# Kernel optimization log

Measured on AMD Instinct MI355X. Metric: run time of the kernel, lower is better.

## Reference

```python
import jax, jax.numpy as jnp
import numpy as np

DIM = 256
HEADS = 8
DIM_HEAD = 32
WS = 8  # window_size
INNER = HEADS * DIM_HEAD
SCALE = DIM_HEAD ** -0.5


def _rel_indices():
    # (WS^2, WS^2, 2) relative position indices, shifted to be non-negative
    idx = np.array([[x, y] for x in range(WS) for y in range(WS)])
    rel = idx[None, :, :] - idx[:, None, :] + (WS - 1)
    return jnp.asarray(rel, dtype=jnp.int32)


def setup_inputs() -> dict:
    key = jax.random.key(0)
    k1, k2, k3, k4 = jax.random.split(key, 4)
    x = jax.random.normal(k1, (2, 4, 128, 128, DIM), dtype=jnp.float32)
    w_qkv = jax.random.normal(k2, (DIM, 3 * INNER), dtype=jnp.float32) * 0.02
    pos_emb = jax.random.normal(k3, (2 * WS - 1, 2 * WS - 1), dtype=jnp.float32)
    w_out = jax.random.normal(k4, (INNER, DIM), dtype=jnp.float32) * 0.02
    b_out = jnp.zeros((DIM,), dtype=jnp.float32)
    return {"x": x, "w_qkv": w_qkv, "pos_emb": pos_emb, "w_out": w_out, "b_out": b_out}


def reference(x, w_qkv, pos_emb, w_out, b_out):
    B, L, H, W, C = x.shape
    nh, nw = H // WS, W // WS
    qkv = x @ w_qkv  # (B,L,H,W,3*INNER)
    q, k, v = jnp.split(qkv, 3, axis=-1)

    def to_windows(t):
        # (B,L,H,W,INNER) -> (B,L,m,nh*nw,WS*WS,DIM_HEAD)
        t = t.reshape(B, L, nh, WS, nw, WS, HEADS, DIM_HEAD)
        t = t.transpose(0, 1, 6, 2, 4, 3, 5, 7)
        return t.reshape(B, L, HEADS, nh * nw, WS * WS, DIM_HEAD)

    q, k, v = to_windows(q), to_windows(k), to_windows(v)

    rel = _rel_indices()
    bias = pos_emb[rel[..., 0], rel[..., 1]]  # (WS^2, WS^2)

    dots = jnp.einsum('blmhic,blmhjc->blmhij', q, k) * SCALE + bias
    attn = jax.nn.softmax(dots, axis=-1)
    out = jnp.einsum('blmhij,blmhjc->blmhic', attn, v)

    # inverse window rearrange: (B,L,m,nh*nw,WS*WS,c) -> (B,L,H,W,INNER)
    out = out.reshape(B, L, HEADS, nh, nw, WS, WS, DIM_HEAD)
    out = out.transpose(0, 1, 3, 5, 4, 6, 2, 7).reshape(B, L, H, W, INNER)
    return out @ w_out + b_out
```

## Files before the change

kernel.cpp:

```cpp
#include <hip/hip_runtime.h>
#include <hip/hip_bf16.h>


typedef __attribute__((ext_vector_type(8))) short bf16x8;
typedef __attribute__((ext_vector_type(4))) float f32x4;

__device__ __forceinline__ f32x4 mfma16(bf16x8 a, bf16x8 b, f32x4 c) {
  return __builtin_amdgcn_mfma_f32_16x16x32_bf16(a, b, c, 0, 0, 0);
}

__device__ __forceinline__ unsigned short f2bf(float f) {
  __hip_bfloat16 h = __float2bfloat16(f);
  return *reinterpret_cast<unsigned short*>(&h);
}

__device__ __forceinline__ uint2 pack4(float a, float b, float c, float d) {
  union { unsigned short u[4]; uint2 v; } pk;
  pk.u[0] = f2bf(a); pk.u[1] = f2bf(b); pk.u[2] = f2bf(c); pk.u[3] = f2bf(d);
  return pk.v;
}

#define LOG2E 1.4426950408889634f
#define EXPSCALE (0.17677669529663687f * 1.4426950408889634f)

#define XO  264
#define RTS 40
#define PS  72
#define RT_ELEMS 1280
#define OFF_RT 16896
#define SMEM_ELTS 22016

__global__ void prep_kernel(const float* __restrict__ w_qkv,
                            const float* __restrict__ w_out,
                            const float* __restrict__ pos_emb,
                            unsigned short* __restrict__ wqkvT,
                            unsigned short* __restrict__ woutT,
                            float* __restrict__ bias64) {
  const int stride = gridDim.x * blockDim.x;
  const int tid = blockIdx.x * blockDim.x + threadIdx.x;
  for (int i = tid; i < 768 * 256; i += stride) {
    int n = i >> 8, k = i & 255;
    int off = ((((n >> 4) * 8 + (k >> 5)) * 4 + ((k >> 3) & 3)) * 16 + (n & 15)) * 8 + (k & 7);
    wqkvT[off] = f2bf(w_qkv[k * 768 + n]);
  }
  for (int i = tid; i < 256 * 256; i += stride) {
    int n = i >> 8, k = i & 255;
    int off = ((((n >> 4) * 8 + (k >> 5)) * 4 + ((k >> 3) & 3)) * 16 + (n & 15)) * 8 + (k & 7);
    woutT[off] = f2bf(w_out[k * 256 + n]);
  }
  for (int i = tid; i < 64 * 64; i += stride) {
    int a = i >> 6, b = i & 63;
    int d0 = (b >> 3) - (a >> 3) + 7;
    int d1 = (b & 7) - (a & 7) + 7;
    bias64[i] = pos_emb[d0 * 15 + d1] * LOG2E;
  }
}

template <bool SWAP>
__device__ __forceinline__ void gemm32(f32x4 (&acc)[4][2],
                                       const unsigned short* __restrict__ a_lds,
                                       const unsigned short* __restrict__ wT,
                                       int col0, int l15, int lq) {
  const f32x4 zero4 = {0.f, 0.f, 0.f, 0.f};
#pragma unroll
  for (int rt = 0; rt < 4; ++rt)
#pragma unroll
    for (int ct = 0; ct < 2; ++ct) acc[rt][ct] = zero4;
#pragma unroll
  for (int kk = 0; kk < 8; ++kk) {
    bf16x8 a[4], b[2];
#pragma unroll
    for (int rt = 0; rt < 4; ++rt)
      a[rt] = *(const bf16x8*)&a_lds[(rt * 16 + l15) * XO + kk * 32 + lq * 8];
#pragma unroll
    for (int ct = 0; ct < 2; ++ct)
      b[ct] = *(const bf16x8*)&wT[((((col0 >> 4) + ct) * 8 + kk) * 4 + lq) * 128 + l15 * 8];
#pragma unroll
    for (int rt = 0; rt < 4; ++rt)
#pragma unroll
      for (int ct = 0; ct < 2; ++ct)
        acc[rt][ct] = SWAP ? mfma16(b[ct], a[rt], acc[rt][ct])
                           : mfma16(a[rt], b[ct], acc[rt][ct]);
  }
}

__global__ __launch_bounds__(256, 3)
void winattn_kernel(const float* __restrict__ x,
                    const unsigned short* __restrict__ wqkvT,
                    const unsigned short* __restrict__ woutT,
                    const float* __restrict__ bias64,
                    const float* __restrict__ b_out,
                    float* __restrict__ out) {
  __shared__ unsigned short smem[SMEM_ELTS];

  const int tid = threadIdx.x;
  const int lane = tid & 63;
  const int w = tid >> 6;
  const int l15 = lane & 15;
  const int lq = lane >> 4;

  const int bid = blockIdx.x;
  const int win = bid & 255;
  const int img = bid >> 8;
  const int wy = win >> 4, wx = win & 15;

  unsigned short* x_lds  = smem;
  unsigned short* oh_lds = smem;
  unsigned short* rt_buf = smem + OFF_RT + w * RT_ELEMS;

  const f32x4 zero4 = {0.f, 0.f, 0.f, 0.f};
  const size_t img_base = (size_t)img * 128 * 128 * 256;

  {
#pragma unroll
    for (int r = 0; r < 16; ++r) {
      int p = r * 4 + w;
      const float* src = x + img_base +
          (((size_t)(wy * 8 + (p >> 3)) * 128) + (wx * 8 + (p & 7))) * 256 + lane * 4;
      float4 v4 = *(const float4*)src;
      *(uint2*)&x_lds[p * XO + lane * 4] = pack4(v4.x, v4.y, v4.z, v4.w);
    }
  }
  __syncthreads();

  bf16x8 qf[4][2], kf[4][2], vf[2][2][2];
  {
    f32x4 acc[4][2];
#pragma unroll
    for (int hh = 0; hh < 2; ++hh) {
      gemm32<true>(acc, x_lds, wqkvT, w * 64 + hh * 32, l15, lq);
#pragma unroll
      for (int h2 = 0; h2 < 2; ++h2) {
#pragma unroll
        for (int rr = 0; rr < 2; ++rr)
#pragma unroll
          for (int ct = 0; ct < 2; ++ct)
            *(uint2*)&rt_buf[(rr * 16 + l15) * RTS + ct * 16 + lq * 4] =
                pack4(acc[h2 * 2 + rr][ct][0], acc[h2 * 2 + rr][ct][1],
                      acc[h2 * 2 + rr][ct][2], acc[h2 * 2 + rr][ct][3]);
#pragma unroll
        for (int rr = 0; rr < 2; ++rr)
          qf[h2 * 2 + rr][hh] = *(const bf16x8*)&rt_buf[(rr * 16 + l15) * RTS + lq * 8];
      }
    }
#pragma unroll
    for (int hh = 0; hh < 2; ++hh) {
      gemm32<true>(acc, x_lds, wqkvT, 256 + w * 64 + hh * 32, l15, lq);
#pragma unroll
      for (int h2 = 0; h2 < 2; ++h2) {
#pragma unroll
        for (int rr = 0; rr < 2; ++rr)
#pragma unroll
          for (int ct = 0; ct < 2; ++ct)
            *(uint2*)&rt_buf[(rr * 16 + l15) * RTS + ct * 16 + lq * 4] =
                pack4(acc[h2 * 2 + rr][ct][0], acc[h2 * 2 + rr][ct][1],
                      acc[h2 * 2 + rr][ct][2], acc[h2 * 2 + rr][ct][3]);
#pragma unroll
        for (int rr = 0; rr < 2; ++rr)
          kf[h2 * 2 + rr][hh] = *(const bf16x8*)&rt_buf[(rr * 16 + l15) * RTS + lq * 8];
      }
    }
#pragma unroll
    for (int hh = 0; hh < 2; ++hh) {
      gemm32<false>(acc, x_lds, wqkvT, 512 + w * 64 + hh * 32, l15, lq);
#pragma unroll
      for (int h2 = 0; h2 < 2; ++h2) {
#pragma unroll
        for (int rr = 0; rr < 2; ++rr)
#pragma unroll
          for (int ct = 0; ct < 2; ++ct)
            *(uint2*)&rt_buf[(ct * 16 + l15) * RTS + rr * 16 + lq * 4] =
                pack4(acc[h2 * 2 + rr][ct][0], acc[h2 * 2 + rr][ct][1],
                      acc[h2 * 2 + rr][ct][2], acc[h2 * 2 + rr][ct][3]);
#pragma unroll
        for (int ft = 0; ft < 2; ++ft)
          vf[ft][h2][hh] = *(const bf16x8*)&rt_buf[(ft * 16 + l15) * RTS + lq * 8];
      }
    }
  }
  __syncthreads();

#pragma unroll
  for (int it = 0; it < 4; ++it) {
    f32x4 bias4[4];
#pragma unroll
    for (int jt = 0; jt < 4; ++jt)
      bias4[jt] = *(const f32x4*)&bias64[(it * 16 + l15) * 64 + jt * 16 + lq * 4];
#pragma unroll
    for (int hh = 0; hh < 2; ++hh) {
      f32x4 s[4];
#pragma unroll
      for (int jt = 0; jt < 4; ++jt)
        s[jt] = mfma16(kf[jt][hh], qf[it][hh], zero4);
      float rs = 0.f;
#pragma unroll
      for (int jt = 0; jt < 4; ++jt)
#pragma unroll
        for (int r = 0; r < 4; ++r) {
          s[jt][r] = __builtin_amdgcn_exp2f(s[jt][r] * EXPSCALE + bias4[jt][r]);
          rs += s[jt][r];
        }
      rs += __shfl_xor(rs, 16);
      rs += __shfl_xor(rs, 32);
      const float rinv = __builtin_amdgcn_rcpf(rs);

#pragma unroll
      for (int jt = 0; jt < 4; ++jt)
        *(uint2*)&rt_buf[l15 * PS + jt * 16 + lq * 4] =
            pack4(s[jt][0], s[jt][1], s[jt][2], s[jt][3]);
      const bf16x8 ap0 = *(const bf16x8*)&rt_buf[l15 * PS + lq * 8];
      const bf16x8 ap1 = *(const bf16x8*)&rt_buf[l15 * PS + 32 + lq * 8];

      f32x4 o0 = mfma16(vf[0][0][hh], ap0, zero4);
      o0 = mfma16(vf[0][1][hh], ap1, o0);
      f32x4 o1 = mfma16(vf[1][0][hh], ap0, zero4);
      o1 = mfma16(vf[1][1][hh], ap1, o1);

      *(uint2*)&oh_lds[(it * 16 + l15) * XO + w * 64 + hh * 32 + lq * 4] =
          pack4(o0[0] * rinv, o0[1] * rinv, o0[2] * rinv, o0[3] * rinv);
      *(uint2*)&oh_lds[(it * 16 + l15) * XO + w * 64 + hh * 32 + 16 + lq * 4] =
          pack4(o1[0] * rinv, o1[1] * rinv, o1[2] * rinv, o1[3] * rinv);
    }
  }
  __syncthreads();

  {
    f32x4 ACC[4][4];
#pragma unroll
    for (int rt = 0; rt < 4; ++rt)
#pragma unroll
      for (int ct = 0; ct < 4; ++ct) ACC[rt][ct] = zero4;
#pragma unroll
    for (int kk = 0; kk < 8; ++kk) {
      bf16x8 a[4], b[4];
#pragma unroll
      for (int rt = 0; rt < 4; ++rt)
        a[rt] = *(const bf16x8*)&oh_lds[(rt * 16 + l15) * XO + kk * 32 + lq * 8];
#pragma unroll
      for (int ct = 0; ct < 4; ++ct)
        b[ct] = *(const bf16x8*)&woutT[(((w * 4 + ct) * 8 + kk) * 4 + lq) * 128 + l15 * 8];
#pragma unroll
      for (int rt = 0; rt < 4; ++rt)
#pragma unroll
        for (int ct = 0; ct < 4; ++ct)
          ACC[rt][ct] = mfma16(b[ct], a[rt], ACC[rt][ct]);
    }
#pragma unroll
    for (int rt = 0; rt < 4; ++rt) {
      const int p = rt * 16 + l15;
      float* orow = out + img_base +
          (((size_t)(wy * 8 + (p >> 3)) * 128) + (wx * 8 + (p & 7))) * 256;
#pragma unroll
      for (int ct = 0; ct < 4; ++ct) {
        const int n0 = w * 64 + ct * 16 + lq * 4;
        const f32x4 bo4 = *(const f32x4*)&b_out[n0];
        f32x4 st;
#pragma unroll
        for (int r = 0; r < 4; ++r) st[r] = ACC[rt][ct][r] + bo4[r];
        *(f32x4*)(orow + n0) = st;
      }
    }
  }
}

extern "C" void kernel_launch(void* const* d_in, const int* in_sizes, int n_in,
                              void* d_out, int out_size, void* d_ws, size_t ws_size,
                              hipStream_t stream) {
  const float* x       = (const float*)d_in[0];
  const float* w_qkv   = (const float*)d_in[1];
  const float* pos_emb = (const float*)d_in[2];
  const float* w_out   = (const float*)d_in[3];
  const float* b_out   = (const float*)d_in[4];
  float* out = (float*)d_out;

  unsigned short* wqkvT = (unsigned short*)d_ws;
  unsigned short* woutT = wqkvT + 768 * 256;
  float* bias64 = (float*)(woutT + 256 * 256);

  prep_kernel<<<96, 256, 0, stream>>>(w_qkv, w_out, pos_emb, wqkvT, woutT, bias64);
  winattn_kernel<<<2048, 256, 0, stream>>>(x, wqkvT, woutT, bias64, b_out, out);
}
```

Baseline: 116.6 us.

## Software-pipeline QKV, attention and output-projection stages within each warp

Interleaves the QKV GEMMs with the register-transpose stores of the previous GEMM using two accumulator sets. The attention loop now computes the next tile's scores and softmax while the current P@V runs. The output projection double-buffers its A/B fragment loads one k-step ahead. The goal is to hide LDS and global load latency behind MFMA work, at the cost of more live registers and possibly lower occupancy or spills.

```diff
diff --git a/kernel.cpp b/kernel.cpp
--- a/kernel.cpp
+++ b/kernel.cpp
@@ -124,90 +124,96 @@
   __syncthreads();
 
   bf16x8 qf[4][2], kf[4][2], vf[2][2][2];
+
+#define RT_QK(ACCV, DEST, HH)                                                   \
+  _Pragma("unroll")                                                             \
+  for (int h2 = 0; h2 < 2; ++h2) {                                              \
+    _Pragma("unroll")                                                           \
+    for (int rr = 0; rr < 2; ++rr)                                              \
+      _Pragma("unroll")                                                         \
+      for (int ct = 0; ct < 2; ++ct)                                            \
+        *(uint2*)&rt_buf[(rr * 16 + l15) * RTS + ct * 16 + lq * 4] =            \
+            pack4(ACCV[h2 * 2 + rr][ct][0], ACCV[h2 * 2 + rr][ct][1],           \
+                  ACCV[h2 * 2 + rr][ct][2], ACCV[h2 * 2 + rr][ct][3]);          \
+    _Pragma("unroll")                                                           \
+    for (int rr = 0; rr < 2; ++rr)                                              \
+      DEST[h2 * 2 + rr][HH] =                                                   \
+          *(const bf16x8*)&rt_buf[(rr * 16 + l15) * RTS + lq * 8];              \
+  }
+
+#define RT_V(ACCV, HH)                                                          \
+  _Pragma("unroll")                                                             \
+  for (int h2 = 0; h2 < 2; ++h2) {                                              \
+    _Pragma("unroll")                                                           \
+    for (int rr = 0; rr < 2; ++rr)                                              \
+      _Pragma("unroll")                                                         \
+      for (int ct = 0; ct < 2; ++ct)                                            \
+        *(uint2*)&rt_buf[(ct * 16 + l15) * RTS + rr * 16 + lq * 4] =            \
+            pack4(ACCV[h2 * 2 + rr][ct][0], ACCV[h2 * 2 + rr][ct][1],           \
+                  ACCV[h2 * 2 + rr][ct][2], ACCV[h2 * 2 + rr][ct][3]);          \
+    _Pragma("unroll")                                                           \
+    for (int ft = 0; ft < 2; ++ft)                                              \
+      vf[ft][h2][HH] =                                                          \
+          *(const bf16x8*)&rt_buf[(ft * 16 + l15) * RTS + lq * 8];              \
+  }
+
   {
-    f32x4 acc[4][2];
-#pragma unroll
-    for (int hh = 0; hh < 2; ++hh) {
-      gemm32<true>(acc, x_lds, wqkvT, w * 64 + hh * 32, l15, lq);
-#pragma unroll
-      for (int h2 = 0; h2 < 2; ++h2) {
-#pragma unroll
-        for (int rr = 0; rr < 2; ++rr)
-#pragma unroll
-          for (int ct = 0; ct < 2; ++ct)
-            *(uint2*)&rt_buf[(rr * 16 + l15) * RTS + ct * 16 + lq * 4] =
-                pack4(acc[h2 * 2 + rr][ct][0], acc[h2 * 2 + rr][ct][1],
-                      acc[h2 * 2 + rr][ct][2], acc[h2 * 2 + rr][ct][3]);
-#pragma unroll
-        for (int rr = 0; rr < 2; ++rr)
-          qf[h2 * 2 + rr][hh] = *(const bf16x8*)&rt_buf[(rr * 16 + l15) * RTS + lq * 8];
-      }
-    }
-#pragma unroll
-    for (int hh = 0; hh < 2; ++hh) {
-      gemm32<true>(acc, x_lds, wqkvT, 256 + w * 64 + hh * 32, l15, lq);
-#pragma unroll
-      for (int h2 = 0; h2 < 2; ++h2) {
-#pragma unroll
-        for (int rr = 0; rr < 2; ++rr)
-#pragma unroll
-          for (int ct = 0; ct < 2; ++ct)
-            *(uint2*)&rt_buf[(rr * 16 + l15) * RTS + ct * 16 + lq * 4] =
-                pack4(acc[h2 * 2 + rr][ct][0], acc[h2 * 2 + rr][ct][1],
-                      acc[h2 * 2 + rr][ct][2], acc[h2 * 2 + rr][ct][3]);
-#pragma unroll
-        for (int rr = 0; rr < 2; ++rr)
-          kf[h2 * 2 + rr][hh] = *(const bf16x8*)&rt_buf[(rr * 16 + l15) * RTS + lq * 8];
-      }
-    }
-#pragma unroll
-    for (int hh = 0; hh < 2; ++hh) {
-      gemm32<false>(acc, x_lds, wqkvT, 512 + w * 64 + hh * 32, l15, lq);
-#pragma unroll
-      for (int h2 = 0; h2 < 2; ++h2) {
-#pragma unroll
-        for (int rr = 0; rr < 2; ++rr)
-#pragma unroll
-          for (int ct = 0; ct < 2; ++ct)
-            *(uint2*)&rt_buf[(ct * 16 + l15) * RTS + rr * 16 + lq * 4] =
-                pack4(acc[h2 * 2 + rr][ct][0], acc[h2 * 2 + rr][ct][1],
-                      acc[h2 * 2 + rr][ct][2], acc[h2 * 2 + rr][ct][3]);
-#pragma unroll
-        for (int ft = 0; ft < 2; ++ft)
-          vf[ft][h2][hh] = *(const bf16x8*)&rt_buf[(ft * 16 + l15) * RTS + lq * 8];
-      }
-    }
+    f32x4 accA[4][2], accB[4][2];
+    gemm32<true >(accA, x_lds, wqkvT,       w * 64 +  0, l15, lq);
+    gemm32<true >(accB, x_lds, wqkvT, 256 + w * 64 +  0, l15, lq);
+    RT_QK(accA, qf, 0)
+    gemm32<true >(accA, x_lds, wqkvT,       w * 64 + 32, l15, lq);
+    RT_QK(accB, kf, 0)
+    gemm32<true >(accB, x_lds, wqkvT, 256 + w * 64 + 32, l15, lq);
+    RT_QK(accA, qf, 1)
+    gemm32<false>(accA, x_lds, wqkvT, 512 + w * 64 +  0, l15, lq);
+    RT_QK(accB, kf, 1)
+    gemm32<false>(accB, x_lds, wqkvT, 512 + w * 64 + 32, l15, lq);
+    RT_V(accA, 0)
+    RT_V(accB, 1)
   }
   __syncthreads();
 
-#pragma unroll
-  for (int it = 0; it < 4; ++it) {
-    f32x4 bias4[4];
-#pragma unroll
-    for (int jt = 0; jt < 4; ++jt)
-      bias4[jt] = *(const f32x4*)&bias64[(it * 16 + l15) * 64 + jt * 16 + lq * 4];
-#pragma unroll
-    for (int hh = 0; hh < 2; ++hh) {
-      f32x4 s[4];
-#pragma unroll
-      for (int jt = 0; jt < 4; ++jt)
-        s[jt] = mfma16(kf[jt][hh], qf[it][hh], zero4);
-      float rs = 0.f;
-#pragma unroll
-      for (int jt = 0; jt < 4; ++jt)
-#pragma unroll
-        for (int r = 0; r < 4; ++r) {
-          s[jt][r] = __builtin_amdgcn_exp2f(s[jt][r] * EXPSCALE + bias4[jt][r]);
-          rs += s[jt][r];
-        }
-      rs += __shfl_xor(rs, 16);
-      rs += __shfl_xor(rs, 32);
-      const float rinv = __builtin_amdgcn_rcpf(rs);
-
+#define COMPUTE_S(IT, HH, SV, RV)                                               \
+  {                                                                             \
+    f32x4 bias4[4];                                                             \
+    _Pragma("unroll")                                                           \
+    for (int jt = 0; jt < 4; ++jt)                                              \
+      bias4[jt] = *(const f32x4*)&bias64[((IT) * 16 + l15) * 64 + jt * 16 + lq * 4]; \
+    float rs = 0.f;                                                             \
+    _Pragma("unroll")                                                           \
+    for (int jt = 0; jt < 4; ++jt) {                                            \
+      SV[jt] = mfma16(kf[jt][HH], qf[IT][HH], zero4);                           \
+      _Pragma("unroll")                                                         \
+      for (int r = 0; r < 4; ++r) {                                             \
+        SV[jt][r] = __builtin_amdgcn_exp2f(SV[jt][r] * EXPSCALE + bias4[jt][r]);\
+        rs += SV[jt][r];                                                        \
+      }                                                                         \
+    }                                                                           \
+    rs += __shfl_xor(rs, 16);                                                   \
+    rs += __shfl_xor(rs, 32);                                                   \
+    RV = __builtin_amdgcn_rcpf(rs);                                             \
+  }
+
+  {
+    f32x4 s[4];
+    float rinv;
+    COMPUTE_S(0, 0, s, rinv)
+#pragma unroll
+    for (int i = 0; i < 8; ++i) {
+      const int it = i >> 1, hh = i & 1;
 #pragma unroll
       for (int jt = 0; jt < 4; ++jt)
         *(uint2*)&rt_buf[l15 * PS + jt * 16 + lq * 4] =
             pack4(s[jt][0], s[jt][1], s[jt][2], s[jt][3]);
+
+      f32x4 sn[4];
+      float rinvn = 0.f;
+      if (i < 7) {
+        const int itn = (i + 1) >> 1, hhn = (i + 1) & 1;
+        COMPUTE_S(itn, hhn, sn, rinvn)
+      }
+
       const bf16x8 ap0 = *(const bf16x8*)&rt_buf[l15 * PS + lq * 8];
       const bf16x8 ap1 = *(const bf16x8*)&rt_buf[l15 * PS + 32 + lq * 8];
 
@@ -220,6 +226,12 @@
           pack4(o0[0] * rinv, o0[1] * rinv, o0[2] * rinv, o0[3] * rinv);
       *(uint2*)&oh_lds[(it * 16 + l15) * XO + w * 64 + hh * 32 + 16 + lq * 4] =
           pack4(o1[0] * rinv, o1[1] * rinv, o1[2] * rinv, o1[3] * rinv);
+
+      if (i < 7) {
+#pragma unroll
+        for (int jt = 0; jt < 4; ++jt) s[jt] = sn[jt];
+        rinv = rinvn;
+      }
     }
   }
   __syncthreads();
@@ -230,21 +242,33 @@
     for (int rt = 0; rt < 4; ++rt)
 #pragma unroll
       for (int ct = 0; ct < 4; ++ct) ACC[rt][ct] = zero4;
+
+    bf16x8 ag[2][4], bg[2][4];
+#pragma unroll
+    for (int rt = 0; rt < 4; ++rt)
+      ag[0][rt] = *(const bf16x8*)&oh_lds[(rt * 16 + l15) * XO + lq * 8];
+#pragma unroll
+    for (int ct = 0; ct < 4; ++ct)
+      bg[0][ct] = *(const bf16x8*)&woutT[(((w * 4 + ct) * 8 + 0) * 4 + lq) * 128 + l15 * 8];
+
 #pragma unroll
     for (int kk = 0; kk < 8; ++kk) {
-      bf16x8 a[4], b[4];
+      const int c = kk & 1, n = c ^ 1;
+      if (kk < 7) {
+#pragma unroll
+        for (int rt = 0; rt < 4; ++rt)
+          ag[n][rt] = *(const bf16x8*)&oh_lds[(rt * 16 + l15) * XO + (kk + 1) * 32 + lq * 8];
+#pragma unroll
+        for (int ct = 0; ct < 4; ++ct)
+          bg[n][ct] = *(const bf16x8*)&woutT[(((w * 4 + ct) * 8 + kk + 1) * 4 + lq) * 128 + l15 * 8];
+      }
 #pragma unroll
       for (int rt = 0; rt < 4; ++rt)
-        a[rt] = *(const bf16x8*)&oh_lds[(rt * 16 + l15) * XO + kk * 32 + lq * 8];
-#pragma unroll
-      for (int ct = 0; ct < 4; ++ct)
-        b[ct] = *(const bf16x8*)&woutT[(((w * 4 + ct) * 8 + kk) * 4 + lq) * 128 + l15 * 8];
-#pragma unroll
-      for (int rt = 0; rt < 4; ++rt)
 #pragma unroll
         for (int ct = 0; ct < 4; ++ct)
-          ACC[rt][ct] = mfma16(b[ct], a[rt], ACC[rt][ct]);
+          ACC[rt][ct] = mfma16(bg[c][ct], ag[c][rt], ACC[rt][ct]);
     }
+
 #pragma unroll
     for (int rt = 0; rt < 4; ++rt) {
       const int p = rt * 16 + l15;
```

New measurement: 132.3 us. 13.5% more time.

## Use eight waves per window block, one attention head per wave

Applied to the files above, without the earlier changes.

The block grows from 4 to 8 waves, so each wave handles one head (32 QKV columns per projection, 32 output columns) instead of two. Per-wave register arrays are halved and the x staging loop is split across 8 waves. More waves per window are meant to give more latency hiding and parallelism per CU. LDS grows to hold 8 per-wave scratch buffers, and launch bounds change to 512 threads, which may limit how many blocks fit on a CU.

```diff
diff --git a/kernel.cpp b/kernel.cpp
--- a/kernel.cpp
+++ b/kernel.cpp
@@ -28,7 +28,7 @@
 #define PS  72
 #define RT_ELEMS 1280
 #define OFF_RT 16896
-#define SMEM_ELTS 22016
+#define SMEM_ELTS 27136
 
 __global__ void prep_kernel(const float* __restrict__ w_qkv,
                             const float* __restrict__ w_out,
@@ -84,7 +84,7 @@
   }
 }
 
-__global__ __launch_bounds__(256, 3)
+__global__ __launch_bounds__(512, 4)
 void winattn_kernel(const float* __restrict__ x,
                     const unsigned short* __restrict__ wqkvT,
                     const unsigned short* __restrict__ woutT,
@@ -113,8 +113,8 @@
 
   {
 #pragma unroll
-    for (int r = 0; r < 16; ++r) {
-      int p = r * 4 + w;
+    for (int r = 0; r < 8; ++r) {
+      int p = r * 8 + w;
       const float* src = x + img_base +
           (((size_t)(wy * 8 + (p >> 3)) * 128) + (wx * 8 + (p & 7))) * 256 + lane * 4;
       float4 v4 = *(const float4*)src;
@@ -123,59 +123,50 @@
   }
   __syncthreads();
 
-  bf16x8 qf[4][2], kf[4][2], vf[2][2][2];
+  bf16x8 qf[4], kf[4], vf[2][2];
   {
     f32x4 acc[4][2];
-#pragma unroll
-    for (int hh = 0; hh < 2; ++hh) {
-      gemm32<true>(acc, x_lds, wqkvT, w * 64 + hh * 32, l15, lq);
-#pragma unroll
-      for (int h2 = 0; h2 < 2; ++h2) {
-#pragma unroll
-        for (int rr = 0; rr < 2; ++rr)
-#pragma unroll
-          for (int ct = 0; ct < 2; ++ct)
-            *(uint2*)&rt_buf[(rr * 16 + l15) * RTS + ct * 16 + lq * 4] =
-                pack4(acc[h2 * 2 + rr][ct][0], acc[h2 * 2 + rr][ct][1],
-                      acc[h2 * 2 + rr][ct][2], acc[h2 * 2 + rr][ct][3]);
-#pragma unroll
-        for (int rr = 0; rr < 2; ++rr)
-          qf[h2 * 2 + rr][hh] = *(const bf16x8*)&rt_buf[(rr * 16 + l15) * RTS + lq * 8];
-      }
-    }
-#pragma unroll
-    for (int hh = 0; hh < 2; ++hh) {
-      gemm32<true>(acc, x_lds, wqkvT, 256 + w * 64 + hh * 32, l15, lq);
-#pragma unroll
-      for (int h2 = 0; h2 < 2; ++h2) {
-#pragma unroll
-        for (int rr = 0; rr < 2; ++rr)
-#pragma unroll
-          for (int ct = 0; ct < 2; ++ct)
-            *(uint2*)&rt_buf[(rr * 16 + l15) * RTS + ct * 16 + lq * 4] =
-                pack4(acc[h2 * 2 + rr][ct][0], acc[h2 * 2 + rr][ct][1],
-                      acc[h2 * 2 + rr][ct][2], acc[h2 * 2 + rr][ct][3]);
-#pragma unroll
-        for (int rr = 0; rr < 2; ++rr)
-          kf[h2 * 2 + rr][hh] = *(const bf16x8*)&rt_buf[(rr * 16 + l15) * RTS + lq * 8];
-      }
-    }
-#pragma unroll
-    for (int hh = 0; hh < 2; ++hh) {
-      gemm32<false>(acc, x_lds, wqkvT, 512 + w * 64 + hh * 32, l15, lq);
-#pragma unroll
-      for (int h2 = 0; h2 < 2; ++h2) {
-#pragma unroll
-        for (int rr = 0; rr < 2; ++rr)
-#pragma unroll
-          for (int ct = 0; ct < 2; ++ct)
-            *(uint2*)&rt_buf[(ct * 16 + l15) * RTS + rr * 16 + lq * 4] =
-                pack4(acc[h2 * 2 + rr][ct][0], acc[h2 * 2 + rr][ct][1],
-                      acc[h2 * 2 + rr][ct][2], acc[h2 * 2 + rr][ct][3]);
-#pragma unroll
-        for (int ft = 0; ft < 2; ++ft)
-          vf[ft][h2][hh] = *(const bf16x8*)&rt_buf[(ft * 16 + l15) * RTS + lq * 8];
-      }
+    gemm32<true>(acc, x_lds, wqkvT, w * 32, l15, lq);
+#pragma unroll
+    for (int h2 = 0; h2 < 2; ++h2) {
+#pragma unroll
+      for (int rr = 0; rr < 2; ++rr)
+#pragma unroll
+        for (int ct = 0; ct < 2; ++ct)
+          *(uint2*)&rt_buf[(rr * 16 + l15) * RTS + ct * 16 + lq * 4] =
+              pack4(acc[h2 * 2 + rr][ct][0], acc[h2 * 2 + rr][ct][1],
+                    acc[h2 * 2 + rr][ct][2], acc[h2 * 2 + rr][ct][3]);
+#pragma unroll
+      for (int rr = 0; rr < 2; ++rr)
+        qf[h2 * 2 + rr] = *(const bf16x8*)&rt_buf[(rr * 16 + l15) * RTS + lq * 8];
+    }
+    gemm32<true>(acc, x_lds, wqkvT, 256 + w * 32, l15, lq);
+#pragma unroll
+    for (int h2 = 0; h2 < 2; ++h2) {
+#pragma unroll
+      for (int rr = 0; rr < 2; ++rr)
+#pragma unroll
+        for (int ct = 0; ct < 2; ++ct)
+          *(uint2*)&rt_buf[(rr * 16 + l15) * RTS + ct * 16 + lq * 4] =
+              pack4(acc[h2 * 2 + rr][ct][0], acc[h2 * 2 + rr][ct][1],
+                    acc[h2 * 2 + rr][ct][2], acc[h2 * 2 + rr][ct][3]);
+#pragma unroll
+      for (int rr = 0; rr < 2; ++rr)
+        kf[h2 * 2 + rr] = *(const bf16x8*)&rt_buf[(rr * 16 + l15) * RTS + lq * 8];
+    }
+    gemm32<false>(acc, x_lds, wqkvT, 512 + w * 32, l15, lq);
+#pragma unroll
+    for (int h2 = 0; h2 < 2; ++h2) {
+#pragma unroll
+      for (int rr = 0; rr < 2; ++rr)
+#pragma unroll
+        for (int ct = 0; ct < 2; ++ct)
+          *(uint2*)&rt_buf[(ct * 16 + l15) * RTS + rr * 16 + lq * 4] =
+              pack4(acc[h2 * 2 + rr][ct][0], acc[h2 * 2 + rr][ct][1],
+                    acc[h2 * 2 + rr][ct][2], acc[h2 * 2 + rr][ct][3]);
+#pragma unroll
+      for (int ft = 0; ft < 2; ++ft)
+        vf[ft][h2] = *(const bf16x8*)&rt_buf[(ft * 16 + l15) * RTS + lq * 8];
     }
   }
   __syncthreads();
@@ -186,63 +177,60 @@
 #pragma unroll
     for (int jt = 0; jt < 4; ++jt)
       bias4[jt] = *(const f32x4*)&bias64[(it * 16 + l15) * 64 + jt * 16 + lq * 4];
-#pragma unroll
-    for (int hh = 0; hh < 2; ++hh) {
-      f32x4 s[4];
-#pragma unroll
-      for (int jt = 0; jt < 4; ++jt)
-        s[jt] = mfma16(kf[jt][hh], qf[it][hh], zero4);
-      float rs = 0.f;
-#pragma unroll
-      for (int jt = 0; jt < 4; ++jt)
-#pragma unroll
-        for (int r = 0; r < 4; ++r) {
-          s[jt][r] = __builtin_amdgcn_exp2f(s[jt][r] * EXPSCALE + bias4[jt][r]);
-          rs += s[jt][r];
-        }
-      rs += __shfl_xor(rs, 16);
-      rs += __shfl_xor(rs, 32);
-      const float rinv = __builtin_amdgcn_rcpf(rs);
-
-#pragma unroll
-      for (int jt = 0; jt < 4; ++jt)
-        *(uint2*)&rt_buf[l15 * PS + jt * 16 + lq * 4] =
-            pack4(s[jt][0], s[jt][1], s[jt][2], s[jt][3]);
-      const bf16x8 ap0 = *(const bf16x8*)&rt_buf[l15 * PS + lq * 8];
-      const bf16x8 ap1 = *(const bf16x8*)&rt_buf[l15 * PS + 32 + lq * 8];
-
-      f32x4 o0 = mfma16(vf[0][0][hh], ap0, zero4);
-      o0 = mfma16(vf[0][1][hh], ap1, o0);
-      f32x4 o1 = mfma16(vf[1][0][hh], ap0, zero4);
-      o1 = mfma16(vf[1][1][hh], ap1, o1);
-
-      *(uint2*)&oh_lds[(it * 16 + l15) * XO + w * 64 + hh * 32 + lq * 4] =
-          pack4(o0[0] * rinv, o0[1] * rinv, o0[2] * rinv, o0[3] * rinv);
-      *(uint2*)&oh_lds[(it * 16 + l15) * XO + w * 64 + hh * 32 + 16 + lq * 4] =
-          pack4(o1[0] * rinv, o1[1] * rinv, o1[2] * rinv, o1[3] * rinv);
-    }
+    f32x4 s[4];
+#pragma unroll
+    for (int jt = 0; jt < 4; ++jt)
+      s[jt] = mfma16(kf[jt], qf[it], zero4);
+    float rs = 0.f;
+#pragma unroll
+    for (int jt = 0; jt < 4; ++jt)
+#pragma unroll
+      for (int r = 0; r < 4; ++r) {
+        s[jt][r] = __builtin_amdgcn_exp2f(s[jt][r] * EXPSCALE + bias4[jt][r]);
+        rs += s[jt][r];
+      }
+    rs += __shfl_xor(rs, 16);
+    rs += __shfl_xor(rs, 32);
+    const float rinv = __builtin_amdgcn_rcpf(rs);
+
+#pragma unroll
+    for (int jt = 0; jt < 4; ++jt)
+      *(uint2*)&rt_buf[l15 * PS + jt * 16 + lq * 4] =
+          pack4(s[jt][0], s[jt][1], s[jt][2], s[jt][3]);
+    const bf16x8 ap0 = *(const bf16x8*)&rt_buf[l15 * PS + lq * 8];
+    const bf16x8 ap1 = *(const bf16x8*)&rt_buf[l15 * PS + 32 + lq * 8];
+
+    f32x4 o0 = mfma16(vf[0][0], ap0, zero4);
+    o0 = mfma16(vf[0][1], ap1, o0);
+    f32x4 o1 = mfma16(vf[1][0], ap0, zero4);
+    o1 = mfma16(vf[1][1], ap1, o1);
+
+    *(uint2*)&oh_lds[(it * 16 + l15) * XO + w * 32 + lq * 4] =
+        pack4(o0[0] * rinv, o0[1] * rinv, o0[2] * rinv, o0[3] * rinv);
+    *(uint2*)&oh_lds[(it * 16 + l15) * XO + w * 32 + 16 + lq * 4] =
+        pack4(o1[0] * rinv, o1[1] * rinv, o1[2] * rinv, o1[3] * rinv);
   }
   __syncthreads();
 
   {
-    f32x4 ACC[4][4];
+    f32x4 ACC[4][2];
 #pragma unroll
     for (int rt = 0; rt < 4; ++rt)
 #pragma unroll
-      for (int ct = 0; ct < 4; ++ct) ACC[rt][ct] = zero4;
+      for (int ct = 0; ct < 2; ++ct) ACC[rt][ct] = zero4;
 #pragma unroll
     for (int kk = 0; kk < 8; ++kk) {
-      bf16x8 a[4], b[4];
+      bf16x8 a[4], b[2];
 #pragma unroll
       for (int rt = 0; rt < 4; ++rt)
         a[rt] = *(const bf16x8*)&oh_lds[(rt * 16 + l15) * XO + kk * 32 + lq * 8];
 #pragma unroll
-      for (int ct = 0; ct < 4; ++ct)
-        b[ct] = *(const bf16x8*)&woutT[(((w * 4 + ct) * 8 + kk) * 4 + lq) * 128 + l15 * 8];
+      for (int ct = 0; ct < 2; ++ct)
+        b[ct] = *(const bf16x8*)&woutT[(((w * 2 + ct) * 8 + kk) * 4 + lq) * 128 + l15 * 8];
 #pragma unroll
       for (int rt = 0; rt < 4; ++rt)
 #pragma unroll
-        for (int ct = 0; ct < 4; ++ct)
+        for (int ct = 0; ct < 2; ++ct)
           ACC[rt][ct] = mfma16(b[ct], a[rt], ACC[rt][ct]);
     }
 #pragma unroll
@@ -251,8 +239,8 @@
       float* orow = out + img_base +
           (((size_t)(wy * 8 + (p >> 3)) * 128) + (wx * 8 + (p & 7))) * 256;
 #pragma unroll
-      for (int ct = 0; ct < 4; ++ct) {
-        const int n0 = w * 64 + ct * 16 + lq * 4;
+      for (int ct = 0; ct < 2; ++ct) {
+        const int n0 = w * 32 + ct * 16 + lq * 4;
         const f32x4 bo4 = *(const f32x4*)&b_out[n0];
         f32x4 st;
 #pragma unroll
@@ -278,5 +266,5 @@
   float* bias64 = (float*)(woutT + 256 * 256);
 
   prep_kernel<<<96, 256, 0, stream>>>(w_qkv, w_out, pos_emb, wqkvT, woutT, bias64);
-  winattn_kernel<<<2048, 256, 0, stream>>>(x, wqkvT, woutT, bias64, b_out, out);
-}
+  winattn_kernel<<<2048, 512, 0, stream>>>(x, wqkvT, woutT, bias64, b_out, out);
+}
```

Result: slower. 126.7 us (+8.7%).
